# Kernel optimization log

Measured on AMD Instinct MI355X. Metric: run time of the kernel, lower is better.

## Reference

```python
import jax, jax.numpy as jnp
import numpy as np
from jax import lax

WINDOW_SIZE = 11
SIGMA = 1.5
RGB_RANGE = 1.0
K1, K2 = 0.01, 0.03
CHANNELS = 3


def gaussian_window(window_size, sigma, channels, dtype=jnp.float32):
    coords = jnp.arange(window_size, dtype=dtype) - window_size // 2
    g = jnp.exp(-(coords ** 2) / (2.0 * sigma * sigma))
    g = g / g.sum()
    w2d = jnp.outer(g, g)
    w2d = w2d / w2d.sum()
    # depthwise kernel: (C, 1, ws, ws) in OIHW with feature_group_count=C
    return jnp.broadcast_to(w2d, (channels, 1, window_size, window_size)).astype(dtype)


def _dwconv(inp, window, padding):
    # depthwise conv2d, groups = C
    C = inp.shape[1]
    return lax.conv_general_dilated(
        inp, window,
        window_strides=(1, 1),
        padding=[(padding, padding), (padding, padding)],
        feature_group_count=C,
        dimension_numbers=('NCHW', 'OIHW', 'NCHW'))


def setup_inputs() -> dict:
    key = jax.random.key(0)
    kx, ky = jax.random.split(key)
    B, C, H, W = 16, CHANNELS, 512, 512
    x = jax.random.uniform(kx, (B, C, H, W), dtype=jnp.float32)
    y = jax.random.uniform(ky, (B, C, H, W), dtype=jnp.float32)
    window = gaussian_window(WINDOW_SIZE, SIGMA, C)
    return {"x": x, "y": y, "window": window}


def reference(x, y, window):
    padding = WINDOW_SIZE // 2
    mu_x = _dwconv(x, window, padding)
    mu_y = _dwconv(y, window, padding)
    mu_x2 = mu_x * mu_x
    mu_y2 = mu_y * mu_y
    mu_xy = mu_x * mu_y
    sigma_x2 = _dwconv(x * x, window, padding) - mu_x2
    sigma_y2 = _dwconv(y * y, window, padding) - mu_y2
    sigma_xy = _dwconv(x * y, window, padding) - mu_xy
    L = RGB_RANGE
    C1 = (K1 * L) ** 2
    C2 = (K2 * L) ** 2
    ssim_map = ((2.0 * mu_xy + C1) * (2.0 * sigma_xy + C2)) / (
        (mu_x2 + mu_y2 + C1) * (sigma_x2 + sigma_y2 + C2) + 1e-12)
    loss = 1.0 - ssim_map
    return loss.mean()
```

## Files before the change

kernel.cpp:

```cpp
#include <hip/hip_runtime.h>


typedef __fp16 f16x8 __attribute__((ext_vector_type(8)));
typedef float f32x4 __attribute__((ext_vector_type(4)));
typedef unsigned u32x4 __attribute__((ext_vector_type(4)));

__device__ __forceinline__ unsigned pk2(float a, float b) {
    return __builtin_bit_cast(unsigned, __builtin_amdgcn_cvt_pkrtz(a, b));
}
__device__ __forceinline__ f32x4 mfma16(f16x8 a, f16x8 b, f32x4 c) {
    return __builtin_amdgcn_mfma_f32_16x16x32_f16(a, b, c, 0, 0, 0);
}

#define SXW 24
#define HRP 40

__global__ __launch_bounds__(256, 6) void ssim_main(
    const float* __restrict__ xg, const float* __restrict__ yg,
    const float* __restrict__ w2d, float* __restrict__ part)
{
    __shared__ __align__(16) unsigned sx[80 * SXW];
    __shared__ __align__(16) unsigned sy[80 * SXW];
    __shared__ __align__(16) unsigned hq[2][32 * HRP];
    __shared__ float tb[12 * 16];
    __shared__ float gsf[12];
    __shared__ float wred[4];

    const int tid = threadIdx.x;

    if (tid < 12) {
        float s = 0.0f;
        if (tid < 11) {
            #pragma unroll
            for (int j = 0; j < 11; ++j) s += w2d[tid * 11 + j];
        }
        gsf[tid] = s;
    }

    const int nwg = 128 * (int)gridDim.z;
    const int flat = (int)blockIdx.x + 16 * ((int)blockIdx.y + 8 * (int)blockIdx.z);
    const int swz = (flat & 7) * (nwg >> 3) + (flat >> 3);
    const int bx = swz & 15, by = (swz >> 4) & 7, bz = swz >> 7;

    const int x0 = bx * 32 - 8;
    const int y0 = by * 64 - 9;
    const size_t zoff = (size_t)bz * (512 * 512);
    const float* __restrict__ xp = xg + zoff;
    const float* __restrict__ yp = yg + zoff;

    const bool interior = (x0 >= 0) & (x0 + 47 < 512) & (y0 >= 0) & (y0 + 79 < 512);
    if (interior) {
        for (int it = tid; it < 80 * 12; it += 256) {
            const int r = it / 12, c4 = it - r * 12;
            const int o = (y0 + r) * 512 + x0 + 4 * c4;
            const float4 vx = *(const float4*)&xp[o];
            const float4 vy = *(const float4*)&yp[o];
            *(uint2*)&sx[2 * it] = make_uint2(pk2(vx.x, vx.y), pk2(vx.z, vx.w));
            *(uint2*)&sy[2 * it] = make_uint2(pk2(vy.x, vy.y), pk2(vy.z, vy.w));
        }
    } else {
        for (int it = tid; it < 80 * 12; it += 256) {
            const int r = it / 12, c4 = it - r * 12;
            const int gr = y0 + r, gc0 = x0 + 4 * c4;
            const bool rok = (unsigned)gr < 512u;
            float xv[4], yv[4];
            #pragma unroll
            for (int j = 0; j < 4; ++j) {
                const int gc = gc0 + j;
                const bool ok = rok & ((unsigned)gc < 512u);
                const int o = gr * 512 + gc;
                xv[j] = ok ? xp[o] : 0.f;
                yv[j] = ok ? yp[o] : 0.f;
            }
            *(uint2*)&sx[2 * it] = make_uint2(pk2(xv[0], xv[1]), pk2(xv[2], xv[3]));
            *(uint2*)&sy[2 * it] = make_uint2(pk2(yv[0], yv[1]), pk2(yv[2], yv[3]));
        }
    }
    __syncthreads();

    if (tid < 192) {
        const int t = tid >> 4;
        float ssum = 0.0f;
        #pragma unroll
        for (int k = 0; k < 11; ++k)
            if (k != 5) ssum += (float)(__fp16)gsf[k];
        const float ccf = (float)(__fp16)(1.0f - ssum);
        const float tv = (float)(__fp16)gsf[t];
        tb[tid] = (t == 5) ? ccf : tv;
    }
    __syncthreads();

    const int lane = tid & 63, wv = tid >> 6;
    const int lm = lane & 15, lg = lane >> 4;

    f16x8 bt, afr;
    {
        const int j = lm ^ ((lg & 1) << 3);
        #pragma unroll
        for (int e = 0; e < 8; ++e) {
            const int k = 8 * lg + e;
            const unsigned t1 = (unsigned)(k - lm - 3);
            const unsigned t2 = (unsigned)(k - lm - 4);
            const unsigned u1 = t1 <= 11u ? t1 : 11u;
            const unsigned u2 = t2 <= 11u ? t2 : 11u;
            bt[e]  = (__fp16)tb[16 * u1 + j];
            afr[e] = (__fp16)tb[16 * u2 + j];
        }
    }

    const bool v2 = (wv < 2);
    auto ldpair = [&](int i, f16x8& xa, f16x8& ya) {
        const int b = i >> 1, tl = i & 1;
        const int sbase = (16 * b + lm) * SXW + 8 * tl + 4 * lg;
        xa = __builtin_bit_cast(f16x8, *(const u32x4*)&sx[sbase]);
        ya = __builtin_bit_cast(f16x8, *(const u32x4*)&sy[sbase]);
    };
    f16x8 xa0, ya0, xa1, ya1, xa2, ya2;
    ldpair(wv,     xa0, ya0);
    ldpair(wv + 4, xa1, ya1);
    ldpair(v2 ? wv + 8 : wv, xa2, ya2);

    f32x4 acc[2][5];
    #pragma unroll
    for (int ch = 0; ch < 2; ++ch)
        #pragma unroll
        for (int q = 0; q < 5; ++q)
            acc[ch][q] = (f32x4){0.f, 0.f, 0.f, 0.f};

    const int rpb = 8 * wv;

    #pragma unroll
    for (int chunk = 0; chunk < 3; ++chunk) {
        auto bitem = [&](const f16x8& xa, const f16x8& ya, int i, bool valid) {
            if (!valid) return;
            const int b = i >> 1, tl = i & 1;
            const f32x4 z4 = {0.f, 0.f, 0.f, 0.f};
            f32x4 d0 = z4, d1 = z4;
            if (chunk == 0)      { d0 = mfma16(xa, bt, z4);      d1 = mfma16(ya, bt, z4); }
            else if (chunk == 1) { d0 = mfma16(xa * xa, bt, z4); d1 = mfma16(ya * ya, bt, z4); }
            else                 { d0 = mfma16(xa * ya, bt, z4); }
            const int ob = (16 * tl + lm) * HRP + 8 * b + 2 * lg;
            *(uint2*)&hq[0][ob] = make_uint2(pk2(d0[0], d0[1]), pk2(d0[2], d0[3]));
            if (chunk < 2)
                *(uint2*)&hq[1][ob] = make_uint2(pk2(d1[0], d1[1]), pk2(d1[2], d1[3]));
        };
        bitem(xa0, ya0, wv,     true);
        bitem(xa1, ya1, wv + 4, true);
        bitem(xa2, ya2, wv + 8, v2);
        __syncthreads();

        #pragma unroll
        for (int ch = 0; ch < 2; ++ch) {
            const int cb = (16 * ch + lm) * HRP + rpb + 4 * lg;
            #pragma unroll
            for (int s = 0; s < 2; ++s) {
                if (chunk == 2 && s == 1) continue;
                const u32x4 w4 = *(const u32x4*)&hq[s][cb];
                acc[ch][2 * chunk + s] =
                    mfma16(afr, __builtin_bit_cast(f16x8, w4), acc[ch][2 * chunk + s]);
            }
        }
        if (chunk < 2) __syncthreads();
    }

    float lsum = 0.0f;
    const float C1 = 1e-4f, C2 = 9e-4f;
    #pragma unroll
    for (int ch = 0; ch < 2; ++ch) {
        #pragma unroll
        for (int r = 0; r < 4; ++r) {
            const float mx = acc[ch][0][r], my = acc[ch][1][r];
            const float exx = acc[ch][2][r], eyy = acc[ch][3][r];
            const float exy = acc[ch][4][r];
            const float mx2 = mx * mx, my2 = my * my, mxy = mx * my;
            const float vx = exx - mx2, vy = eyy - my2, vxy = exy - mxy;
            const float num = (2.0f * mxy + C1) * (2.0f * vxy + C2);
            const float den = (mx2 + my2 + C1) * (vx + vy + C2) + 1e-12f;
            lsum = fmaf(num, __builtin_amdgcn_rcpf(den), lsum);
        }
    }

    #pragma unroll
    for (int off = 32; off > 0; off >>= 1)
        lsum += __shfl_down(lsum, off, 64);
    if ((tid & 63) == 0) wred[tid >> 6] = lsum;
    __syncthreads();
    if (tid == 0) part[swz] = wred[0] + wred[1] + wred[2] + wred[3];
}

__global__ __launch_bounds__(256) void ssim_reduce(
    const float* __restrict__ part, float* __restrict__ out,
    int n, float invN)
{
    __shared__ float wred[4];
    float s = 0.0f;
    for (int i = threadIdx.x; i < n; i += 256) s += part[i];
    #pragma unroll
    for (int off = 32; off > 0; off >>= 1)
        s += __shfl_down(s, off, 64);
    if ((threadIdx.x & 63) == 0) wred[threadIdx.x >> 6] = s;
    __syncthreads();
    if (threadIdx.x == 0)
        out[0] = 1.0f - (wred[0] + wred[1] + wred[2] + wred[3]) * invN;
}

extern "C" void kernel_launch(void* const* d_in, const int* in_sizes, int n_in,
                              void* d_out, int out_size, void* d_ws, size_t ws_size,
                              hipStream_t stream) {
    const float* x   = (const float*)d_in[0];
    const float* y   = (const float*)d_in[1];
    const float* w2d = (const float*)d_in[2];
    float* out  = (float*)d_out;
    float* part = (float*)d_ws;

    const int H = 512, W = 512;
    const int total = in_sizes[0];
    const int Z = total / (H * W);

    dim3 grid(W / 32, H / 64, Z);
    const int nblk = (W / 32) * (H / 64) * Z;
    ssim_main<<<grid, 256, 0, stream>>>(x, y, w2d, part);

    const float invN = 1.0f / (float)total;
    ssim_reduce<<<1, 256, 0, stream>>>(part, out, nblk, invN);
}
```

Measured before the change: 144.9 us.

## Use 512-thread blocks splitting column halves across waves, pack filter taps

Doubles the workgroup to 512 threads so each wave handles one 16-column half of the output instead of both, leaving one band item per wave plus two extra waves covering the leftover band. Filter fragments are now built from a packed fp16 pair table with vector loads instead of per-element gathers. This gives more waves per tile for latency hiding and fewer registers per wave, at the cost of duplicated horizontal-pass work distribution and more barrier participants.

```diff
diff --git a/kernel.cpp b/kernel.cpp
--- a/kernel.cpp
+++ b/kernel.cpp
@@ -15,16 +15,16 @@
 #define SXW 24
 #define HRP 40
 
-__global__ __launch_bounds__(256, 6) void ssim_main(
+__global__ __launch_bounds__(512, 8) void ssim_main(
     const float* __restrict__ xg, const float* __restrict__ yg,
     const float* __restrict__ w2d, float* __restrict__ part)
 {
     __shared__ __align__(16) unsigned sx[80 * SXW];
     __shared__ __align__(16) unsigned sy[80 * SXW];
     __shared__ __align__(16) unsigned hq[2][32 * HRP];
-    __shared__ float tb[12 * 16];
+    __shared__ unsigned tbp[64];
     __shared__ float gsf[12];
-    __shared__ float wred[4];
+    __shared__ float wred[8];
 
     const int tid = threadIdx.x;
 
@@ -50,7 +50,7 @@
 
     const bool interior = (x0 >= 0) & (x0 + 47 < 512) & (y0 >= 0) & (y0 + 79 < 512);
     if (interior) {
-        for (int it = tid; it < 80 * 12; it += 256) {
+        for (int it = tid; it < 80 * 12; it += 512) {
             const int r = it / 12, c4 = it - r * 12;
             const int o = (y0 + r) * 512 + x0 + 4 * c4;
             const float4 vx = *(const float4*)&xp[o];
@@ -59,7 +59,7 @@
             *(uint2*)&sy[2 * it] = make_uint2(pk2(vy.x, vy.y), pk2(vy.z, vy.w));
         }
     } else {
-        for (int it = tid; it < 80 * 12; it += 256) {
+        for (int it = tid; it < 80 * 12; it += 512) {
             const int r = it / 12, c4 = it - r * 12;
             const int gr = y0 + r, gc0 = x0 + 4 * c4;
             const bool rok = (unsigned)gr < 512u;
@@ -78,15 +78,20 @@
     }
     __syncthreads();
 
-    if (tid < 192) {
-        const int t = tid >> 4;
+    if (tid < 64) {
         float ssum = 0.0f;
         #pragma unroll
         for (int k = 0; k < 11; ++k)
             if (k != 5) ssum += (float)(__fp16)gsf[k];
-        const float ccf = (float)(__fp16)(1.0f - ssum);
-        const float tv = (float)(__fp16)gsf[t];
-        tb[tid] = (t == 5) ? ccf : tv;
+        const __fp16 cc = (__fp16)(1.0f - ssum);
+        auto tap = [&](int t) -> __fp16 {
+            if ((unsigned)t > 10u) return (__fp16)0.f;
+            return (t == 5) ? cc : (__fp16)gsf[t];
+        };
+        const int t = tid - 19;
+        const unsigned short lo = __builtin_bit_cast(unsigned short, tap(t));
+        const unsigned short hi = __builtin_bit_cast(unsigned short, tap(t + 1));
+        tbp[tid] = (unsigned)lo | ((unsigned)hi << 16);
     }
     __syncthreads();
 
@@ -95,44 +100,36 @@
 
     f16x8 bt, afr;
     {
-        const int j = lm ^ ((lg & 1) << 3);
+        const int k0 = 8 * lg - lm + 16;
+        u32x4 wb, wa;
         #pragma unroll
-        for (int e = 0; e < 8; ++e) {
-            const int k = 8 * lg + e;
-            const unsigned t1 = (unsigned)(k - lm - 3);
-            const unsigned t2 = (unsigned)(k - lm - 4);
-            const unsigned u1 = t1 <= 11u ? t1 : 11u;
-            const unsigned u2 = t2 <= 11u ? t2 : 11u;
-            bt[e]  = (__fp16)tb[16 * u1 + j];
-            afr[e] = (__fp16)tb[16 * u2 + j];
-        }
-    }
-
-    const bool v2 = (wv < 2);
+        for (int i = 0; i < 4; ++i) {
+            wb[i] = tbp[k0 + 2 * i];
+            wa[i] = tbp[k0 - 1 + 2 * i];
+        }
+        bt  = __builtin_bit_cast(f16x8, wb);
+        afr = __builtin_bit_cast(f16x8, wa);
+    }
+
     auto ldpair = [&](int i, f16x8& xa, f16x8& ya) {
         const int b = i >> 1, tl = i & 1;
         const int sbase = (16 * b + lm) * SXW + 8 * tl + 4 * lg;
         xa = __builtin_bit_cast(f16x8, *(const u32x4*)&sx[sbase]);
         ya = __builtin_bit_cast(f16x8, *(const u32x4*)&sy[sbase]);
     };
-    f16x8 xa0, ya0, xa1, ya1, xa2, ya2;
-    ldpair(wv,     xa0, ya0);
-    ldpair(wv + 4, xa1, ya1);
-    ldpair(v2 ? wv + 8 : wv, xa2, ya2);
-
-    f32x4 acc[2][5];
-    #pragma unroll
-    for (int ch = 0; ch < 2; ++ch)
-        #pragma unroll
-        for (int q = 0; q < 5; ++q)
-            acc[ch][q] = (f32x4){0.f, 0.f, 0.f, 0.f};
-
-    const int rpb = 8 * wv;
+    f16x8 xa0, ya0;
+    ldpair(wv, xa0, ya0);
+
+    f32x4 acc[5];
+    #pragma unroll
+    for (int q = 0; q < 5; ++q) acc[q] = (f32x4){0.f, 0.f, 0.f, 0.f};
+
+    const int rq = wv >> 1, ch = wv & 1;
+    const int rpb = 8 * rq;
 
     #pragma unroll
     for (int chunk = 0; chunk < 3; ++chunk) {
-        auto bitem = [&](const f16x8& xa, const f16x8& ya, int i, bool valid) {
-            if (!valid) return;
+        auto bitem = [&](const f16x8& xa, const f16x8& ya, int i) {
             const int b = i >> 1, tl = i & 1;
             const f32x4 z4 = {0.f, 0.f, 0.f, 0.f};
             f32x4 d0 = z4, d1 = z4;
@@ -144,20 +141,22 @@
             if (chunk < 2)
                 *(uint2*)&hq[1][ob] = make_uint2(pk2(d1[0], d1[1]), pk2(d1[2], d1[3]));
         };
-        bitem(xa0, ya0, wv,     true);
-        bitem(xa1, ya1, wv + 4, true);
-        bitem(xa2, ya2, wv + 8, v2);
+        bitem(xa0, ya0, wv);
+        if (wv < 2) {
+            f16x8 xf, yf;
+            ldpair(wv + 8, xf, yf);
+            bitem(xf, yf, wv + 8);
+        }
         __syncthreads();
 
-        #pragma unroll
-        for (int ch = 0; ch < 2; ++ch) {
+        {
             const int cb = (16 * ch + lm) * HRP + rpb + 4 * lg;
             #pragma unroll
             for (int s = 0; s < 2; ++s) {
                 if (chunk == 2 && s == 1) continue;
                 const u32x4 w4 = *(const u32x4*)&hq[s][cb];
-                acc[ch][2 * chunk + s] =
-                    mfma16(afr, __builtin_bit_cast(f16x8, w4), acc[ch][2 * chunk + s]);
+                acc[2 * chunk + s] =
+                    mfma16(afr, __builtin_bit_cast(f16x8, w4), acc[2 * chunk + s]);
             }
         }
         if (chunk < 2) __syncthreads();
@@ -166,18 +165,15 @@
     float lsum = 0.0f;
     const float C1 = 1e-4f, C2 = 9e-4f;
     #pragma unroll
-    for (int ch = 0; ch < 2; ++ch) {
-        #pragma unroll
-        for (int r = 0; r < 4; ++r) {
-            const float mx = acc[ch][0][r], my = acc[ch][1][r];
-            const float exx = acc[ch][2][r], eyy = acc[ch][3][r];
-            const float exy = acc[ch][4][r];
-            const float mx2 = mx * mx, my2 = my * my, mxy = mx * my;
-            const float vx = exx - mx2, vy = eyy - my2, vxy = exy - mxy;
-            const float num = (2.0f * mxy + C1) * (2.0f * vxy + C2);
-            const float den = (mx2 + my2 + C1) * (vx + vy + C2) + 1e-12f;
-            lsum = fmaf(num, __builtin_amdgcn_rcpf(den), lsum);
-        }
+    for (int r = 0; r < 4; ++r) {
+        const float mx = acc[0][r], my = acc[1][r];
+        const float exx = acc[2][r], eyy = acc[3][r];
+        const float exy = acc[4][r];
+        const float mx2 = mx * mx, my2 = my * my, mxy = mx * my;
+        const float vx = exx - mx2, vy = eyy - my2, vxy = exy - mxy;
+        const float num = (2.0f * mxy + C1) * (2.0f * vxy + C2);
+        const float den = (mx2 + my2 + C1) * (vx + vy + C2) + 1e-12f;
+        lsum = fmaf(num, __builtin_amdgcn_rcpf(den), lsum);
     }
 
     #pragma unroll
@@ -185,7 +181,12 @@
         lsum += __shfl_down(lsum, off, 64);
     if ((tid & 63) == 0) wred[tid >> 6] = lsum;
     __syncthreads();
-    if (tid == 0) part[swz] = wred[0] + wred[1] + wred[2] + wred[3];
+    if (tid == 0) {
+        float s = 0.0f;
+        #pragma unroll
+        for (int w = 0; w < 8; ++w) s += wred[w];
+        part[swz] = s;
+    }
 }
 
 __global__ __launch_bounds__(256) void ssim_reduce(
@@ -219,7 +220,7 @@
 
     dim3 grid(W / 32, H / 64, Z);
     const int nblk = (W / 32) * (H / 64) * Z;
-    ssim_main<<<grid, 256, 0, stream>>>(x, y, w2d, part);
+    ssim_main<<<grid, 512, 0, stream>>>(x, y, w2d, part);
 
     const float invN = 1.0f / (float)total;
     ssim_reduce<<<1, 256, 0, stream>>>(part, out, nblk, invN);
```

After: 145.9 us. No clear change (+0.7%).
